# Performance work log

Measured on AMD Instinct MI355X. Metric: run time of the kernel, lower is better.

The kernel has to match this reference:

```python
import jax, jax.numpy as jnp
import numpy as np

L, B, H, P = 2048, 16, 512, 256
EPS = 1e-6  # flax nnx LayerNorm default


def setup_inputs() -> dict:
    key = jax.random.key(0)
    ks = jax.random.split(key, 12)
    x = jax.random.normal(ks[0], (L, B, H), jnp.float32)
    d = jax.random.bernoulli(ks[1], 0.01, (L, B))  # sparse reset signal
    hidden_re = jnp.zeros((1, B, P), jnp.float32)
    hidden_im = jnp.zeros((1, B, P), jnp.float32)
    # S5 diagonal state matrix (stable: Re < 0)
    Lambda_re = -0.5 * jnp.exp(0.5 * jax.random.normal(ks[2], (P,), jnp.float32))
    Lambda_im = np.float32(np.pi) * jax.random.normal(ks[3], (P,), jnp.float32)
    B_re = jax.random.normal(ks[4], (P, H), jnp.float32) / np.sqrt(2.0 * H).astype(np.float32)
    B_im = jax.random.normal(ks[5], (P, H), jnp.float32) / np.sqrt(2.0 * H).astype(np.float32)
    C_re = jax.random.normal(ks[6], (H, P), jnp.float32) / np.sqrt(P).astype(np.float32)
    C_im = jax.random.normal(ks[7], (H, P), jnp.float32) / np.sqrt(P).astype(np.float32)
    D = jax.random.normal(ks[8], (H,), jnp.float32)
    log_step = jax.random.uniform(ks[9], (P,), jnp.float32,
                                  minval=np.log(1e-3).astype(np.float32),
                                  maxval=np.log(1e-1).astype(np.float32))
    ln_scale = jnp.ones((H,), jnp.float32)
    ln_bias = jnp.zeros((H,), jnp.float32)
    out2_w = jax.random.normal(ks[10], (H, H), jnp.float32) / np.sqrt(H).astype(np.float32)
    out2_b = jnp.zeros((H,), jnp.float32)
    return dict(x=x, d=d, hidden_re=hidden_re, hidden_im=hidden_im,
                Lambda_re=Lambda_re, Lambda_im=Lambda_im, B_re=B_re, B_im=B_im,
                C_re=C_re, C_im=C_im, D=D, log_step=log_step,
                ln_scale=ln_scale, ln_bias=ln_bias, out2_w=out2_w, out2_b=out2_b)


def reference(x, d, hidden_re, hidden_im, Lambda_re, Lambda_im, B_re, B_im,
              C_re, C_im, D, log_step, ln_scale, ln_bias, out2_w, out2_b):
    def ln(v):
        mu = v.mean(-1, keepdims=True)
        var = v.var(-1, keepdims=True)
        return (v - mu) * jax.lax.rsqrt(var + EPS) * ln_scale + ln_bias

    skip = x
    xn = ln(x)  # prenorm

    # --- S5 SSM (ZOH discretization), vmapped over batch == vectorized over axis 1 ---
    step = jnp.exp(log_step)  # step_rescale = 1.0
    Lam = (Lambda_re + 1j * Lambda_im).astype(jnp.complex64)          # (P,)
    Lam_bar = jnp.exp(Lam * step.astype(jnp.complex64))                # (P,)
    B_bar = ((Lam_bar - 1.0) / Lam)[:, None] * (B_re + 1j * B_im).astype(jnp.complex64)  # (P,H)
    Bu = jnp.einsum('lbh,ph->lbp', xn.astype(jnp.complex64), B_bar)    # (L,B,P)

    keep = (1.0 - d.astype(jnp.float32)).astype(jnp.complex64)         # reset zeroes the carry
    a = Lam_bar[None, None, :] * keep[:, :, None]                      # (L,B,P)
    h0 = (hidden_re + 1j * hidden_im).astype(jnp.complex64)[0]         # (B,P)
    Bu = Bu.at[0].add(a[0] * h0)                                       # fold in initial hidden

    def binop(e1, e2):
        a1, b1 = e1
        a2, b2 = e2
        return (a2 * a1, a2 * b1 + b2)

    _, xs = jax.lax.associative_scan(binop, (a, Bu), axis=0)           # (L,B,P) states
    Cmat = (C_re + 1j * C_im).astype(jnp.complex64)
    ys = 2.0 * jnp.einsum('lbp,hp->lbh', xs, Cmat).real + D * xn       # conj-sym readout + feedthrough
    new_hidden = xs[-1:]                                               # (1,B,P)

    y = ln(ys)  # gtrxl norm (shared LayerNorm)
    # half_glu2: x * sigmoid(W2 gelu(x) + b2)
    x1 = jax.nn.gelu(y)  # approximate=True matches nnx.gelu
    y = y * jax.nn.sigmoid(x1 @ out2_w + out2_b)
    out = skip + y
    return (new_hidden.real, new_hidden.imag, out)
```

## Files before the change

kernel.cpp:

```cpp
#include <hip/hip_runtime.h>

#define LL 2048
#define BB 16
#define HH 512
#define PP 256
#define MM (LL*BB)
#define NN 512
#define KK 512
#define NC 64
#define CLEN 32
#define NKT (KK/64)

typedef __bf16 bf16x8 __attribute__((ext_vector_type(8)));
typedef float  f32x4  __attribute__((ext_vector_type(4)));

__device__ __forceinline__ unsigned short f2bf(float f) {
  unsigned u = __builtin_bit_cast(unsigned, f);
  u = (u + 0x7fffu + ((u >> 16) & 1u)) >> 16;
  return (unsigned short)u;
}
__device__ __forceinline__ float bf2f(unsigned short s) {
  unsigned u = ((unsigned)s) << 16;
  return __builtin_bit_cast(float, u);
}

__global__ void detect_kernel(const unsigned int* __restrict__ dw, int* __restrict__ flag) {
  __shared__ int sInt, sFloat;
  if (threadIdx.x == 0) { sInt = 1; sFloat = 1; }
  __syncthreads();
  int allInt = 1, allFloat = 1;
  for (int i = threadIdx.x; i < 8192; i += 256) {
    unsigned v = dw[i];
    if (v > 1u) allInt = 0;
    if (v != 0u && v != 0x3f800000u) allFloat = 0;
  }
  if (!allInt) atomicAnd(&sInt, 0);
  if (!allFloat) atomicAnd(&sFloat, 0);
  __syncthreads();
  if (threadIdx.x == 0) *flag = sInt ? 0 : (sFloat ? 1 : 2);
}

__device__ __forceinline__ float keep_val(const void* d, int flag, int idx) {
  if (flag == 0) return 1.f - (float)((const int*)d)[idx];
  if (flag == 1) return 1.f - ((const float*)d)[idx];
  return 1.f - (float)((const unsigned char*)d)[idx];
}

__global__ void precompute_kernel(
    const float* __restrict__ Lre, const float* __restrict__ Lim,
    const float* __restrict__ Bre, const float* __restrict__ Bim,
    const float* __restrict__ Cre, const float* __restrict__ Cim,
    const float* __restrict__ lstep, const float* __restrict__ w2,
    unsigned short* __restrict__ W1t, unsigned short* __restrict__ W2t,
    unsigned short* __restrict__ W3t, float* __restrict__ lam_re,
    float* __restrict__ lam_im) {
  int t = blockIdx.x * 256 + threadIdx.x;
  int k = t & (KK - 1);
  int n = t >> 9;
  {
    int p = n & (PP - 1);
    float lr = Lre[p], li = Lim[p];
    float st = expf(lstep[p]);
    float er = expf(lr * st);
    float ang = li * st;
    float lbr = er * cosf(ang), lbi = er * sinf(ang);
    float den = lr * lr + li * li;
    float wr = ((lbr - 1.f) * lr + lbi * li) / den;
    float wi = (lbi * lr - (lbr - 1.f) * li) / den;
    float br = Bre[p * HH + k], bi = Bim[p * HH + k];
    float v = (n < PP) ? (wr * br - wi * bi) : (wr * bi + wi * br);
    W1t[(size_t)n * KK + k] = f2bf(v);
  }
  {
    float v = (k < PP) ? (2.f * Cre[n * PP + k]) : (-2.f * Cim[n * PP + (k - PP)]);
    W2t[(size_t)n * KK + k] = f2bf(v);
  }
  W3t[(size_t)n * KK + k] = f2bf(w2[(size_t)k * HH + n]);
  if (t < PP) {
    float lr = Lre[t], li = Lim[t];
    float st = expf(lstep[t]);
    float er = expf(lr * st);
    float ang = li * st;
    lam_re[t] = er * cosf(ang);
    lam_im[t] = er * sinf(ang);
  }
}

__global__ void ln1_kernel(const float* __restrict__ x, const float* __restrict__ sc,
                           const float* __restrict__ bs, unsigned short* __restrict__ xn) {
  int row = blockIdx.x * 4 + (threadIdx.x >> 6);
  int lane = threadIdx.x & 63;
  const float4* xr = (const float4*)(x + (size_t)row * HH) + lane * 2;
  float4 a = xr[0], b = xr[1];
  float s = (a.x + a.y) + (a.z + a.w) + (b.x + b.y) + (b.z + b.w);
  float q = a.x * a.x + a.y * a.y + a.z * a.z + a.w * a.w +
            b.x * b.x + b.y * b.y + b.z * b.z + b.w * b.w;
#pragma unroll
  for (int off = 32; off; off >>= 1) { s += __shfl_xor(s, off); q += __shfl_xor(q, off); }
  float mean = s * (1.f / HH);
  float var = fmaxf(q * (1.f / HH) - mean * mean, 0.f);
  float rstd = rsqrtf(var + 1e-6f);
  const float4* scp = (const float4*)sc + lane * 2;
  const float4* bsp = (const float4*)bs + lane * 2;
  float4 s0 = scp[0], s1 = scp[1], b0 = bsp[0], b1 = bsp[1];
  unsigned short o[8];
  o[0] = f2bf((a.x - mean) * rstd * s0.x + b0.x);
  o[1] = f2bf((a.y - mean) * rstd * s0.y + b0.y);
  o[2] = f2bf((a.z - mean) * rstd * s0.z + b0.z);
  o[3] = f2bf((a.w - mean) * rstd * s0.w + b0.w);
  o[4] = f2bf((b.x - mean) * rstd * s1.x + b1.x);
  o[5] = f2bf((b.y - mean) * rstd * s1.y + b1.y);
  o[6] = f2bf((b.z - mean) * rstd * s1.z + b1.z);
  o[7] = f2bf((b.w - mean) * rstd * s1.w + b1.w);
  uint4 pk;
  pk.x = o[0] | ((unsigned)o[1] << 16);
  pk.y = o[2] | ((unsigned)o[3] << 16);
  pk.z = o[4] | ((unsigned)o[5] << 16);
  pk.w = o[6] | ((unsigned)o[7] << 16);
  *((uint4*)(xn + (size_t)row * HH) + lane) = pk;
}

__global__ void ln2_kernel(const unsigned short* __restrict__ ys, const float* __restrict__ sc,
                           const float* __restrict__ bs, unsigned short* __restrict__ y,
                           unsigned short* __restrict__ x1) {
  int row = blockIdx.x * 4 + (threadIdx.x >> 6);
  int lane = threadIdx.x & 63;
  uint4 pin = *((const uint4*)(ys + (size_t)row * HH) + lane);
  float v[8];
  v[0] = bf2f((unsigned short)(pin.x & 0xffff)); v[1] = bf2f((unsigned short)(pin.x >> 16));
  v[2] = bf2f((unsigned short)(pin.y & 0xffff)); v[3] = bf2f((unsigned short)(pin.y >> 16));
  v[4] = bf2f((unsigned short)(pin.z & 0xffff)); v[5] = bf2f((unsigned short)(pin.z >> 16));
  v[6] = bf2f((unsigned short)(pin.w & 0xffff)); v[7] = bf2f((unsigned short)(pin.w >> 16));
  float s = 0.f, q = 0.f;
#pragma unroll
  for (int j = 0; j < 8; j++) { s += v[j]; q += v[j] * v[j]; }
#pragma unroll
  for (int off = 32; off; off >>= 1) { s += __shfl_xor(s, off); q += __shfl_xor(q, off); }
  float mean = s * (1.f / HH);
  float var = fmaxf(q * (1.f / HH) - mean * mean, 0.f);
  float rstd = rsqrtf(var + 1e-6f);
  const float4* scp = (const float4*)sc + lane * 2;
  const float4* bsp = (const float4*)bs + lane * 2;
  float4 s0 = scp[0], s1 = scp[1], b0 = bsp[0], b1 = bsp[1];
  float scv[8] = { s0.x, s0.y, s0.z, s0.w, s1.x, s1.y, s1.z, s1.w };
  float bsv[8] = { b0.x, b0.y, b0.z, b0.w, b1.x, b1.y, b1.z, b1.w };
  unsigned short oy[8], og[8];
#pragma unroll
  for (int j = 0; j < 8; j++) {
    float yv = (v[j] - mean) * rstd * scv[j] + bsv[j];
    oy[j] = f2bf(yv);
    float g = 0.5f * yv * (1.f + tanhf(0.7978845608f * (yv + 0.044715f * yv * yv * yv)));
    og[j] = f2bf(g);
  }
  uint4 py, pg;
  py.x = oy[0] | ((unsigned)oy[1] << 16); py.y = oy[2] | ((unsigned)oy[3] << 16);
  py.z = oy[4] | ((unsigned)oy[5] << 16); py.w = oy[6] | ((unsigned)oy[7] << 16);
  pg.x = og[0] | ((unsigned)og[1] << 16); pg.y = og[2] | ((unsigned)og[3] << 16);
  pg.z = og[4] | ((unsigned)og[5] << 16); pg.w = og[6] | ((unsigned)og[7] << 16);
  *((uint4*)(y  + (size_t)row * HH) + lane) = py;
  *((uint4*)(x1 + (size_t)row * HH) + lane) = pg;
}

template <int EPI>
__global__ __launch_bounds__(512, 2) void gemm_kernel(
    const unsigned short* __restrict__ A, const unsigned short* __restrict__ Wt,
    void* __restrict__ Cout, const float* __restrict__ Dvec,
    const unsigned short* __restrict__ aux16, const float* __restrict__ skip) {
  extern __shared__ unsigned short smem[];
  const int tid = threadIdx.x;
  const int w = tid >> 6, lane = tid & 63;
  const int wr = w >> 2, wc = w & 3;
  const int l15 = lane & 15, g16 = lane >> 4;
  const int wgid = blockIdx.x;
  const int xcd = wgid & 7, bidx = wgid >> 3;
  const int m0 = (xcd * 16 + (bidx >> 1)) * 256;
  const int n0 = (bidx & 1) * 256;

  const int rS = tid >> 2;
  const int cgS = (tid & 3) ^ ((rS >> 1) & 3);

  auto stageA = [&](int buf, int kh, int kt) {
    const unsigned short* gp = A + (size_t)(m0 + rS) * KK + kt * 64 + kh * 32 + cgS * 8;
    unsigned short* dp = smem + buf * 16384 + kh * 8192 + (w * 64) * 8;
    __builtin_amdgcn_global_load_lds((const __attribute__((address_space(1))) void*)gp,
                                     (__attribute__((address_space(3))) void*)dp, 16, 0, 0);
    __builtin_amdgcn_global_load_lds(
        (const __attribute__((address_space(1))) void*)(gp + (size_t)128 * KK),
        (__attribute__((address_space(3))) void*)(dp + 512 * 8), 16, 0, 0);
  };
  auto stageB = [&](int buf, int kh, int kt) {
    const unsigned short* gp = Wt + (size_t)(n0 + rS) * KK + kt * 64 + kh * 32 + cgS * 8;
    unsigned short* dp = smem + 32768 + buf * 16384 + kh * 8192 + (w * 64) * 8;
    __builtin_amdgcn_global_load_lds((const __attribute__((address_space(1))) void*)gp,
                                     (__attribute__((address_space(3))) void*)dp, 16, 0, 0);
    __builtin_amdgcn_global_load_lds(
        (const __attribute__((address_space(1))) void*)(gp + (size_t)128 * KK),
        (__attribute__((address_space(3))) void*)(dp + 512 * 8), 16, 0, 0);
  };
  auto readA = [&](int buf, int ks, int fm) -> bf16x8 {
    int row = wr * 128 + fm * 16 + l15;
    int ch = g16 ^ ((row >> 1) & 3);
    return *(const bf16x8*)(smem + buf * 16384 + ks * 8192 + row * 32 + ch * 8);
  };
  auto readB = [&](int buf, int ks, int fn) -> bf16x8 {
    int row = wc * 64 + fn * 16 + l15;
    int ch = g16 ^ ((row >> 1) & 3);
    return *(const bf16x8*)(smem + 32768 + buf * 16384 + ks * 8192 + row * 32 + ch * 8);
  };

  f32x4 acc[8][4];
#pragma unroll
  for (int i = 0; i < 8; i++)
#pragma unroll
    for (int j = 0; j < 4; j++) acc[i][j] = (f32x4){0.f, 0.f, 0.f, 0.f};
  bf16x8 bF[4];

#define PHASE(CB, KS, FG, STAGE_STMT, DO_VM)                                    \
  {                                                                             \
    bf16x8 aF[4];                                                               \
    _Pragma("unroll") for (int fi = 0; fi < 4; fi++)                            \
        aF[fi] = readA(CB, KS, (FG)*4 + fi);                                    \
    if ((FG) == 0) {                                                            \
      _Pragma("unroll") for (int fi = 0; fi < 4; fi++) bF[fi] = readB(CB, KS, fi); \
    }                                                                           \
    STAGE_STMT;                                                                 \
    __builtin_amdgcn_s_barrier();                                               \
    asm volatile("s_waitcnt lgkmcnt(0)" ::: "memory");                          \
    __builtin_amdgcn_sched_barrier(0);                                          \
    __builtin_amdgcn_s_setprio(1);                                              \
    _Pragma("unroll") for (int fi = 0; fi < 4; fi++)                            \
      _Pragma("unroll") for (int fj = 0; fj < 4; fj++)                          \
        acc[(FG)*4 + fi][fj] = __builtin_amdgcn_mfma_f32_16x16x32_bf16(         \
            aF[fi], bF[fj], acc[(FG)*4 + fi][fj], 0, 0, 0);                     \
    __builtin_amdgcn_s_setprio(0);                                              \
    if (DO_VM) asm volatile("s_waitcnt vmcnt(8)" ::: "memory");                 \
    __builtin_amdgcn_s_barrier();                                               \
  }

  stageA(0, 0, 0); stageB(0, 0, 0);
  stageA(0, 1, 0); stageB(0, 1, 0);
  stageA(1, 0, 1); stageB(1, 0, 1);
  asm volatile("s_waitcnt vmcnt(8)" ::: "memory");
  __builtin_amdgcn_s_barrier();

  for (int j = 0; j < NKT / 2; ++j) {
    const int t1 = 2 * j + 1;
    const int t2 = (2 * j + 2 < NKT) ? 2 * j + 2 : NKT - 1;
    const int t3 = (2 * j + 3 < NKT) ? 2 * j + 3 : NKT - 1;
    const bool s2 = (2 * j + 2) < NKT, s3 = (2 * j + 3) < NKT;
    PHASE(0, 0, 0, { stageA(1, 1, t1); }, false);
    PHASE(0, 0, 1, { stageB(1, 1, t1); }, true);
    PHASE(0, 1, 0, { if (s2) stageA(0, 0, t2); }, false);
    PHASE(0, 1, 1, { if (s2) stageB(0, 0, t2); }, true);
    PHASE(1, 0, 0, { if (s2) stageA(0, 1, t2); }, false);
    PHASE(1, 0, 1, { if (s2) stageB(0, 1, t2); }, true);
    PHASE(1, 1, 0, { if (s3) stageA(1, 0, t3); }, false);
    PHASE(1, 1, 1, { if (s3) stageB(1, 0, t3); }, true);
  }
#undef PHASE

  const int lr4 = g16 * 4;
#pragma unroll
  for (int fm = 0; fm < 8; fm++) {
    int rowb = m0 + wr * 128 + fm * 16 + lr4;
#pragma unroll
    for (int fn = 0; fn < 4; fn++) {
      int col = n0 + wc * 64 + fn * 16 + l15;
#pragma unroll
      for (int jj = 0; jj < 4; jj++) {
        size_t idxo = (size_t)(rowb + jj) * NN + col;
        float v = acc[fm][fn][jj];
        if (EPI == 0) {
          ((unsigned short*)Cout)[idxo] = f2bf(v);
        } else if (EPI == 1) {
          ((unsigned short*)Cout)[idxo] = f2bf(v + Dvec[col] * bf2f(aux16[idxo]));
        } else {
          float z = v + Dvec[col];
          float sg = 1.f / (1.f + expf(-z));
          ((float*)Cout)[idxo] = skip[idxo] + bf2f(aux16[idxo]) * sg;
        }
      }
    }
  }
}

__global__ void scanA_kernel(const unsigned short* __restrict__ Bu, const void* __restrict__ d,
                             const int* __restrict__ dflag, const float* __restrict__ lam_re,
                             const float* __restrict__ lam_im, float* __restrict__ Ar,
                             float* __restrict__ Ai, float* __restrict__ Sr,
                             float* __restrict__ Si) {
  int bx = blockIdx.x;
  int c = bx >> 4, b = bx & 15;
  int p = threadIdx.x;
  int fl = *dflag;
  float lr = lam_re[p], li = lam_im[p];
  float Apr = 1.f, Api = 0.f, sr = 0.f, si = 0.f;
  int l0 = c * CLEN;
  for (int j = 0; j < CLEN; j++) {
    int l = l0 + j;
    float kp = keep_val(d, fl, l * BB + b);
    float ar = lr * kp, ai = li * kp;
    size_t ro = (size_t)(l * BB + b) * NN;
    float bur = bf2f(Bu[ro + p]), bui = bf2f(Bu[ro + PP + p]);
    float nsr = ar * sr - ai * si + bur;
    float nsi = ar * si + ai * sr + bui;
    sr = nsr; si = nsi;
    float nar = ar * Apr - ai * Api;
    float nai = ar * Api + ai * Apr;
    Apr = nar; Api = nai;
  }
  int o = bx * PP + p;
  Ar[o] = Apr; Ai[o] = Api; Sr[o] = sr; Si[o] = si;
}

__global__ void scanB_kernel(const float* __restrict__ hr0, const float* __restrict__ hi0,
                             const float* __restrict__ Ar, const float* __restrict__ Ai,
                             const float* __restrict__ Sr, const float* __restrict__ Si,
                             float* __restrict__ Cr, float* __restrict__ Ci,
                             float* __restrict__ outHid) {
  int b = blockIdx.x;
  int p = threadIdx.x;
  float cr = hr0[b * PP + p], ci = hi0[b * PP + p];
  for (int c = 0; c < NC; c++) {
    int o = (c * BB + b) * PP + p;
    Cr[o] = cr; Ci[o] = ci;
    float ar = Ar[o], ai = Ai[o];
    float nr = ar * cr - ai * ci + Sr[o];
    float ni = ar * ci + ai * cr + Si[o];
    cr = nr; ci = ni;
  }
  outHid[b * PP + p] = cr;
  outHid[BB * PP + b * PP + p] = ci;
}

__global__ void scanC_kernel(const unsigned short* __restrict__ Bu, const void* __restrict__ d,
                             const int* __restrict__ dflag, const float* __restrict__ lam_re,
                             const float* __restrict__ lam_im, const float* __restrict__ Cr,
                             const float* __restrict__ Ci, unsigned short* __restrict__ xs) {
  int bx = blockIdx.x;
  int c = bx >> 4, b = bx & 15;
  int p = threadIdx.x;
  int fl = *dflag;
  float lr = lam_re[p], li = lam_im[p];
  float hr = Cr[bx * PP + p], hi = Ci[bx * PP + p];
  int l0 = c * CLEN;
  for (int j = 0; j < CLEN; j++) {
    int l = l0 + j;
    float kp = keep_val(d, fl, l * BB + b);
    float ar = lr * kp, ai = li * kp;
    size_t ro = (size_t)(l * BB + b) * NN;
    float bur = bf2f(Bu[ro + p]), bui = bf2f(Bu[ro + PP + p]);
    float nhr = ar * hr - ai * hi + bur;
    float nhi = ar * hi + ai * hr + bui;
    hr = nhr; hi = nhi;
    xs[ro + p] = f2bf(hr);
    xs[ro + PP + p] = f2bf(hi);
  }
}

extern "C" void kernel_launch(void* const* d_in, const int* in_sizes, int n_in,
                              void* d_out, int out_size, void* d_ws, size_t ws_size,
                              hipStream_t stream) {
  const float* x    = (const float*)d_in[0];
  const void*  dmask= d_in[1];
  const float* hidr = (const float*)d_in[2];
  const float* hidi = (const float*)d_in[3];
  const float* Lre  = (const float*)d_in[4];
  const float* Lim  = (const float*)d_in[5];
  const float* Bre  = (const float*)d_in[6];
  const float* Bim  = (const float*)d_in[7];
  const float* Cre  = (const float*)d_in[8];
  const float* Cim  = (const float*)d_in[9];
  const float* Dv   = (const float*)d_in[10];
  const float* lst  = (const float*)d_in[11];
  const float* lsc  = (const float*)d_in[12];
  const float* lbs  = (const float*)d_in[13];
  const float* w2   = (const float*)d_in[14];
  const float* b2   = (const float*)d_in[15];
  float* out = (float*)d_out;

  char* ws = (char*)d_ws;
  size_t off = 0;
  auto alloc = [&](size_t bytes) -> void* {
    void* p = ws + off;
    off += (bytes + 255) & ~(size_t)255;
    return p;
  };
  unsigned short* xn  = (unsigned short*)alloc((size_t)MM * KK * 2);
  unsigned short* xs  = (unsigned short*)alloc((size_t)MM * KK * 2);
  unsigned short* Bu  = (unsigned short*)alloc((size_t)MM * NN * 2);
  unsigned short* W1t = (unsigned short*)alloc((size_t)NN * KK * 2);
  unsigned short* W2t = (unsigned short*)alloc((size_t)NN * KK * 2);
  unsigned short* W3t = (unsigned short*)alloc((size_t)NN * KK * 2);
  float* lam_re = (float*)alloc(PP * 4);
  float* lam_im = (float*)alloc(PP * 4);
  float* Ar = (float*)alloc((size_t)NC * BB * PP * 4);
  float* Ai = (float*)alloc((size_t)NC * BB * PP * 4);
  float* Sr = (float*)alloc((size_t)NC * BB * PP * 4);
  float* Si = (float*)alloc((size_t)NC * BB * PP * 4);
  float* Cr = (float*)alloc((size_t)NC * BB * PP * 4);
  float* Ci = (float*)alloc((size_t)NC * BB * PP * 4);
  int* dflag = (int*)alloc(256);
  unsigned short* y   = xn;
  unsigned short* x1  = xs;
  unsigned short* ysb = Bu;

  hipFuncSetAttribute((const void*)gemm_kernel<0>,
                      hipFuncAttributeMaxDynamicSharedMemorySize, 131072);
  hipFuncSetAttribute((const void*)gemm_kernel<1>,
                      hipFuncAttributeMaxDynamicSharedMemorySize, 131072);
  hipFuncSetAttribute((const void*)gemm_kernel<2>,
                      hipFuncAttributeMaxDynamicSharedMemorySize, 131072);

  detect_kernel<<<1, 256, 0, stream>>>((const unsigned int*)dmask, dflag);
  precompute_kernel<<<1024, 256, 0, stream>>>(Lre, Lim, Bre, Bim, Cre, Cim, lst, w2,
                                              W1t, W2t, W3t, lam_re, lam_im);
  ln1_kernel<<<MM / 4, 256, 0, stream>>>(x, lsc, lbs, xn);
  gemm_kernel<0><<<256, 512, 131072, stream>>>(xn, W1t, Bu, nullptr, nullptr, nullptr);
  scanA_kernel<<<NC * BB, 256, 0, stream>>>(Bu, dmask, dflag, lam_re, lam_im, Ar, Ai, Sr, Si);
  scanB_kernel<<<BB, 256, 0, stream>>>(hidr, hidi, Ar, Ai, Sr, Si, Cr, Ci, out);
  scanC_kernel<<<NC * BB, 256, 0, stream>>>(Bu, dmask, dflag, lam_re, lam_im, Cr, Ci, xs);
  gemm_kernel<1><<<256, 512, 131072, stream>>>(xs, W2t, ysb, Dv, xn, nullptr);
  ln2_kernel<<<MM / 4, 256, 0, stream>>>(ysb, lsc, lbs, y, x1);
  gemm_kernel<2><<<256, 512, 131072, stream>>>(x1, W3t, out + 2 * BB * PP, b2, y, x);
}
```

Before: 199.6 us.

## Use 128x128 GEMM tiles for epilogue GEMMs and stage epilogue stores through LDS

Adds a smaller 128x128-tile GEMM kernel with direct global-to-LDS loads and uses it, at 1024 blocks, for the two GEMMs that carry fused epilogues. Their epilogues now stage results through LDS so the aux, skip and output accesses are vectorised and coalesced. The 256-tile GEMM keeps only the plain bf16 store, now also staged through LDS, and its sched_barrier is removed. The smaller tiles aim for better occupancy and load balance but give less data reuse per tile and a simpler, non-pipelined K loop.

```diff
diff --git a/kernel.cpp b/kernel.cpp
--- a/kernel.cpp
+++ b/kernel.cpp
@@ -162,7 +162,7 @@
 }
 
 template <int EPI>
-__global__ __launch_bounds__(512, 2) void gemm_kernel(
+__global__ __launch_bounds__(512, 2) void gemm256_kernel(
     const unsigned short* __restrict__ A, const unsigned short* __restrict__ Wt,
     void* __restrict__ Cout, const float* __restrict__ Dvec,
     const unsigned short* __restrict__ aux16, const float* __restrict__ skip) {
@@ -226,7 +226,6 @@
     STAGE_STMT;                                                                 \
     __builtin_amdgcn_s_barrier();                                               \
     asm volatile("s_waitcnt lgkmcnt(0)" ::: "memory");                          \
-    __builtin_amdgcn_sched_barrier(0);                                          \
     __builtin_amdgcn_s_setprio(1);                                              \
     _Pragma("unroll") for (int fi = 0; fi < 4; fi++)                            \
       _Pragma("unroll") for (int fj = 0; fj < 4; fj++)                          \
@@ -259,27 +258,179 @@
   }
 #undef PHASE
 
-  const int lr4 = g16 * 4;
-#pragma unroll
-  for (int fm = 0; fm < 8; fm++) {
-    int rowb = m0 + wr * 128 + fm * 16 + lr4;
-#pragma unroll
-    for (int fn = 0; fn < 4; fn++) {
-      int col = n0 + wc * 64 + fn * 16 + l15;
-#pragma unroll
-      for (int jj = 0; jj < 4; jj++) {
-        size_t idxo = (size_t)(rowb + jj) * NN + col;
-        float v = acc[fm][fn][jj];
-        if (EPI == 0) {
-          ((unsigned short*)Cout)[idxo] = f2bf(v);
-        } else if (EPI == 1) {
-          ((unsigned short*)Cout)[idxo] = f2bf(v + Dvec[col] * bf2f(aux16[idxo]));
-        } else {
-          float z = v + Dvec[col];
-          float sg = 1.f / (1.f + expf(-z));
-          ((float*)Cout)[idxo] = skip[idxo] + bf2f(aux16[idxo]) * sg;
+  __syncthreads();
+  unsigned short* lbf = smem;
+#pragma unroll
+  for (int j = 0; j < 4; j++) {
+#pragma unroll
+    for (int h = 0; h < 2; h++) {
+      int fm = 2 * j + h;
+#pragma unroll
+      for (int fn = 0; fn < 4; fn++) {
+        int col = wc * 64 + fn * 16 + l15;
+#pragma unroll
+        for (int jj = 0; jj < 4; jj++) {
+          int lrow = wr * 32 + h * 16 + g16 * 4 + jj;
+          lbf[lrow * 264 + col] = f2bf(acc[fm][fn][jj]);
         }
       }
+    }
+    __syncthreads();
+#pragma unroll
+    for (int sw = 0; sw < 4; sw++) {
+      int lrow = sw * 16 + (tid >> 5);
+      int tc = tid & 31;
+      int grow = m0 + (lrow >> 5) * 128 + (2 * j + ((lrow >> 4) & 1)) * 16 + (lrow & 15);
+      int gcol = n0 + tc * 8;
+      uint4 v = *(const uint4*)&lbf[lrow * 264 + tc * 8];
+      *(uint4*)(((unsigned short*)Cout) + (size_t)grow * NN + gcol) = v;
+    }
+    __syncthreads();
+  }
+}
+
+template <int EPI>
+__global__ __launch_bounds__(256, 4) void gemm128_kernel(
+    const unsigned short* __restrict__ A, const unsigned short* __restrict__ Wt,
+    void* __restrict__ Cout, const float* __restrict__ Dvec,
+    const unsigned short* __restrict__ aux16, const float* __restrict__ skip) {
+  __shared__ char lds[33280];
+  unsigned short* lA = (unsigned short*)lds;
+  unsigned short* lB = (unsigned short*)(lds + 16384);
+  int tid = threadIdx.x;
+  int w = tid >> 6, lane = tid & 63;
+  int wgid = blockIdx.x;
+  int xcd = wgid & 7, bidx = wgid >> 3;
+  int m0 = (xcd * 32 + (bidx >> 2)) * 128;
+  int n0 = (bidx & 3) * 128;
+  int wr = w >> 1, wc = w & 1;
+  const int l15 = lane & 15, g16 = lane >> 4;
+  f32x4 acc[4][4];
+#pragma unroll
+  for (int i = 0; i < 4; i++)
+#pragma unroll
+    for (int j = 0; j < 4; j++) acc[i][j] = (f32x4){0.f, 0.f, 0.f, 0.f};
+
+  for (int kt = 0; kt < NKT; ++kt) {
+    __syncthreads();
+#pragma unroll
+    for (int i = 0; i < 4; i++) {
+      int sidx = i * 256 + tid;
+      int r = sidx >> 3, c = sidx & 7;
+      int cs = c ^ (r & 7);
+      const unsigned short* g = A + (size_t)(m0 + r) * KK + kt * 64 + cs * 8;
+      unsigned short* l = &lA[(i * 256 + w * 64) * 8];
+      __builtin_amdgcn_global_load_lds((const __attribute__((address_space(1))) void*)g,
+                                       (__attribute__((address_space(3))) void*)l, 16, 0, 0);
+    }
+#pragma unroll
+    for (int i = 0; i < 4; i++) {
+      int sidx = i * 256 + tid;
+      int r = sidx >> 3, c = sidx & 7;
+      int cs = c ^ (r & 7);
+      const unsigned short* g = Wt + (size_t)(n0 + r) * KK + kt * 64 + cs * 8;
+      unsigned short* l = &lB[(i * 256 + w * 64) * 8];
+      __builtin_amdgcn_global_load_lds((const __attribute__((address_space(1))) void*)g,
+                                       (__attribute__((address_space(3))) void*)l, 16, 0, 0);
+    }
+    __syncthreads();
+#pragma unroll
+    for (int ks = 0; ks < 2; ++ks) {
+      bf16x8 aF[4], bF[4];
+#pragma unroll
+      for (int m = 0; m < 4; m++) {
+        int row = wr * 64 + m * 16 + l15;
+        int s = ks * 4 + g16;
+        aF[m] = *(const bf16x8*)&lA[row * 64 + (s ^ (row & 7)) * 8];
+      }
+#pragma unroll
+      for (int n = 0; n < 4; n++) {
+        int row = wc * 64 + n * 16 + l15;
+        int s = ks * 4 + g16;
+        bF[n] = *(const bf16x8*)&lB[row * 64 + (s ^ (row & 7)) * 8];
+      }
+#pragma unroll
+      for (int m = 0; m < 4; m++)
+#pragma unroll
+        for (int n = 0; n < 4; n++)
+          acc[m][n] = __builtin_amdgcn_mfma_f32_16x16x32_bf16(aF[m], bF[n], acc[m][n], 0, 0, 0);
+    }
+  }
+  __syncthreads();
+
+  if (EPI == 1) {
+    unsigned short* lbf = (unsigned short*)lds;
+#pragma unroll
+    for (int j = 0; j < 4; j++) {
+#pragma unroll
+      for (int fn = 0; fn < 4; fn++) {
+        int col = wc * 64 + fn * 16 + l15;
+#pragma unroll
+        for (int jj = 0; jj < 4; jj++) {
+          int lrow = wr * 16 + g16 * 4 + jj;
+          lbf[lrow * 136 + col] = f2bf(acc[j][fn][jj]);
+        }
+      }
+      __syncthreads();
+#pragma unroll
+      for (int sw = 0; sw < 2; sw++) {
+        int lrow = sw * 16 + (tid >> 4);
+        int tc = tid & 15;
+        int grow = m0 + (lrow >> 4) * 64 + j * 16 + (lrow & 15);
+        int gcol = n0 + tc * 8;
+        uint4 v = *(const uint4*)&lbf[lrow * 136 + tc * 8];
+        uint4 au = *(const uint4*)(aux16 + (size_t)grow * NN + gcol);
+        float4 d0 = *(const float4*)&Dvec[gcol];
+        float4 d1 = *(const float4*)&Dvec[gcol + 4];
+        unsigned short o[8];
+        unsigned vv[4] = { v.x, v.y, v.z, v.w };
+        unsigned aa[4] = { au.x, au.y, au.z, au.w };
+        float dd[8] = { d0.x, d0.y, d0.z, d0.w, d1.x, d1.y, d1.z, d1.w };
+#pragma unroll
+        for (int e = 0; e < 8; e++) {
+          float av = bf2f((unsigned short)((e & 1) ? (vv[e >> 1] >> 16) : (vv[e >> 1] & 0xffff)));
+          float xu = bf2f((unsigned short)((e & 1) ? (aa[e >> 1] >> 16) : (aa[e >> 1] & 0xffff)));
+          o[e] = f2bf(av + dd[e] * xu);
+        }
+        uint4 pk;
+        pk.x = o[0] | ((unsigned)o[1] << 16); pk.y = o[2] | ((unsigned)o[3] << 16);
+        pk.z = o[4] | ((unsigned)o[5] << 16); pk.w = o[6] | ((unsigned)o[7] << 16);
+        *(uint4*)(((unsigned short*)Cout) + (size_t)grow * NN + gcol) = pk;
+      }
+      __syncthreads();
+    }
+  } else {
+    float* lf = (float*)lds;
+#pragma unroll
+    for (int j = 0; j < 4; j++) {
+#pragma unroll
+      for (int fn = 0; fn < 4; fn++) {
+        int col = wc * 64 + fn * 16 + l15;
+#pragma unroll
+        for (int jj = 0; jj < 4; jj++) {
+          int lrow = wr * 16 + g16 * 4 + jj;
+          lf[lrow * 132 + col] = acc[j][fn][jj];
+        }
+      }
+      __syncthreads();
+#pragma unroll
+      for (int sw = 0; sw < 4; sw++) {
+        int lrow = sw * 8 + (tid >> 5);
+        int tc = tid & 31;
+        int grow = m0 + (lrow >> 4) * 64 + j * 16 + (lrow & 15);
+        int gcol = n0 + tc * 4;
+        float4 v = *(const float4*)&lf[lrow * 132 + tc * 4];
+        float4 d = *(const float4*)&Dvec[gcol];
+        float4 sk = *(const float4*)(skip + (size_t)grow * NN + gcol);
+        ushort4 au = *(const ushort4*)(aux16 + (size_t)grow * NN + gcol);
+        float4 o;
+        o.x = sk.x + bf2f(au.x) / (1.f + expf(-(v.x + d.x)));
+        o.y = sk.y + bf2f(au.y) / (1.f + expf(-(v.y + d.y)));
+        o.z = sk.z + bf2f(au.z) / (1.f + expf(-(v.z + d.z)));
+        o.w = sk.w + bf2f(au.w) / (1.f + expf(-(v.w + d.w)));
+        *(float4*)(((float*)Cout) + (size_t)grow * NN + gcol) = o;
+      }
+      __syncthreads();
     }
   }
 }
@@ -405,22 +556,18 @@
   unsigned short* x1  = xs;
   unsigned short* ysb = Bu;
 
-  hipFuncSetAttribute((const void*)gemm_kernel<0>,
-                      hipFuncAttributeMaxDynamicSharedMemorySize, 131072);
-  hipFuncSetAttribute((const void*)gemm_kernel<1>,
-                      hipFuncAttributeMaxDynamicSharedMemorySize, 131072);
-  hipFuncSetAttribute((const void*)gemm_kernel<2>,
+  hipFuncSetAttribute((const void*)gemm256_kernel<0>,
                       hipFuncAttributeMaxDynamicSharedMemorySize, 131072);
 
   detect_kernel<<<1, 256, 0, stream>>>((const unsigned int*)dmask, dflag);
   precompute_kernel<<<1024, 256, 0, stream>>>(Lre, Lim, Bre, Bim, Cre, Cim, lst, w2,
                                               W1t, W2t, W3t, lam_re, lam_im);
   ln1_kernel<<<MM / 4, 256, 0, stream>>>(x, lsc, lbs, xn);
-  gemm_kernel<0><<<256, 512, 131072, stream>>>(xn, W1t, Bu, nullptr, nullptr, nullptr);
+  gemm256_kernel<0><<<256, 512, 131072, stream>>>(xn, W1t, Bu, nullptr, nullptr, nullptr);
   scanA_kernel<<<NC * BB, 256, 0, stream>>>(Bu, dmask, dflag, lam_re, lam_im, Ar, Ai, Sr, Si);
   scanB_kernel<<<BB, 256, 0, stream>>>(hidr, hidi, Ar, Ai, Sr, Si, Cr, Ci, out);
   scanC_kernel<<<NC * BB, 256, 0, stream>>>(Bu, dmask, dflag, lam_re, lam_im, Cr, Ci, xs);
-  gemm_kernel<1><<<256, 512, 131072, stream>>>(xs, W2t, ysb, Dv, xn, nullptr);
+  gemm128_kernel<1><<<1024, 256, 0, stream>>>(xs, W2t, ysb, Dv, xn, nullptr);
   ln2_kernel<<<MM / 4, 256, 0, stream>>>(ysb, lsc, lbs, y, x1);
-  gemm_kernel<2><<<256, 512, 131072, stream>>>(x1, W3t, out + 2 * BB * PP, b2, y, x);
-}
+  gemm128_kernel<2><<<1024, 256, 0, stream>>>(x1, W3t, out + 2 * BB * PP, b2, y, x);
+}
```

After: 196.4 us. No clear change (-1.6%).
